# Kernel tuning notes

Hardware: AMD Instinct MI355X
Metric: run time of the kernel (lower is better)

The kernel has to match this reference:

```python
import jax, jax.numpy as jnp
import numpy as np

D_MODEL = 512
D_STATE = 64
HEADDIM = 64
EXPAND = 2
D_CONV = 4
D_INNER = EXPAND * D_MODEL            # 1024
NHEADS = D_INNER // HEADDIM           # 16
CONV_DIM = D_INNER + 2 * D_STATE      # 1152 (x, B, C share the depthwise conv)
D_IN_PROJ = 2 * D_INNER + 2 * D_STATE + NHEADS  # z, xBC, dt
C_IN = 512


def setup_inputs() -> dict:
    key = jax.random.key(0)
    ks = jax.random.split(key, 10)
    hs = jax.random.normal(ks[0], (1, C_IN, 16, 16, 16), jnp.float32)
    return {
        "hidden_states": hs,
        # 1x1 conv projections (weight stored as (out,in))
        "proj_in_w": jax.random.normal(ks[1], (D_MODEL, C_IN), jnp.float32) / np.float32(np.sqrt(C_IN)),
        "proj_in_b": jnp.zeros((D_MODEL,), jnp.float32),
        "proj_out_w": jax.random.normal(ks[2], (C_IN, D_MODEL), jnp.float32) * jnp.float32(0.02),
        "proj_out_b": jnp.zeros((C_IN,), jnp.float32),
        # Mamba2 core params
        "in_proj_w": jax.random.normal(ks[3], (D_IN_PROJ, D_MODEL), jnp.float32) / np.float32(np.sqrt(D_MODEL)),
        "conv_w": jax.random.normal(ks[4], (CONV_DIM, D_CONV), jnp.float32) / np.float32(np.sqrt(D_CONV)),
        "conv_b": jnp.zeros((CONV_DIM,), jnp.float32),
        "dt_bias": jnp.log(jnp.expm1(jax.random.uniform(ks[5], (NHEADS,), jnp.float32, 1e-3, 0.1))),
        "A_log": jnp.log(jax.random.uniform(ks[6], (NHEADS,), jnp.float32, 1.0, 16.0)),
        "D": jnp.ones((NHEADS,), jnp.float32),
        "norm_w": jnp.ones((D_INNER,), jnp.float32),
        "out_proj_w": jax.random.normal(ks[7], (D_MODEL, D_INNER), jnp.float32) / np.float32(np.sqrt(D_INNER)),
    }


def _mamba2(x, in_proj_w, conv_w, conv_b, dt_bias, A_log, Dp, norm_w, out_proj_w):
    # x: (N, T, d_model) with N = B*H*W (independent pixel sequences over time)
    N, T, _ = x.shape
    zxbcdt = jnp.einsum('ntd,ed->nte', x, in_proj_w)  # (N,T,D_IN_PROJ)
    z = zxbcdt[..., :D_INNER]
    xBC = zxbcdt[..., D_INNER:D_INNER + CONV_DIM]
    dt = zxbcdt[..., D_INNER + CONV_DIM:]             # (N,T,NHEADS)
    # causal depthwise conv along T (kernel D_CONV, left-padded), then SiLU
    pad = jnp.pad(xBC, ((0, 0), (D_CONV - 1, 0), (0, 0)))
    xc = sum(pad[:, k:k + T, :] * conv_w[:, k] for k in range(D_CONV))
    xBC = jax.nn.silu(xc + conv_b)
    xs = xBC[..., :D_INNER].reshape(N, T, NHEADS, HEADDIM)
    Bm = xBC[..., D_INNER:D_INNER + D_STATE]          # (N,T,D_STATE), ngroups=1
    Cm = xBC[..., D_INNER + D_STATE:]                 # (N,T,D_STATE)
    dt = jax.nn.softplus(dt + dt_bias)                # (N,T,NHEADS)
    A = -jnp.exp(A_log)                               # (NHEADS,)

    def step(h, inp):
        # h: (N, NHEADS, HEADDIM, D_STATE)
        dt_t, x_t, B_t, C_t = inp
        dA = jnp.exp(dt_t * A)                        # (N,NHEADS)
        h = h * dA[:, :, None, None] + (dt_t[:, :, None] * x_t)[..., None] * B_t[:, None, None, :]
        y_t = jnp.einsum('nhps,ns->nhp', h, C_t)      # (N,NHEADS,HEADDIM)
        return h, y_t

    h0 = jnp.zeros((N, NHEADS, HEADDIM, D_STATE), x.dtype)
    _, ys = jax.lax.scan(step, h0, (dt.swapaxes(0, 1), xs.swapaxes(0, 1), Bm.swapaxes(0, 1), Cm.swapaxes(0, 1)))
    y = ys.swapaxes(0, 1) + Dp[None, None, :, None] * xs   # skip term
    # gated RMSNorm: norm(y * silu(z)) * weight
    y = y.reshape(N, T, D_INNER) * jax.nn.silu(z)
    y = y * jax.lax.rsqrt(jnp.mean(y * y, axis=-1, keepdims=True) + 1e-5) * norm_w
    return jnp.einsum('ntd,od->nto', y, out_proj_w)


def reference(hidden_states, proj_in_w, proj_in_b, proj_out_w, proj_out_b,
              in_proj_w, conv_w, conv_b, dt_bias, A_log, D, norm_w, out_proj_w):
    B, C, T, H, W = hidden_states.shape
    # proj_in: 1x1 conv over channels == per-pixel matmul
    x = jnp.einsum('bcthw,dc->bthwd', hidden_states, proj_in_w) + proj_in_b
    # (B,T,H,W,D) -> (B*H*W, T, D): each pixel becomes a temporal sequence
    x = x.transpose(0, 2, 3, 1, 4).reshape(B * H * W, T, D_MODEL)
    y = _mamba2(x, in_proj_w, conv_w, conv_b, dt_bias, A_log, D, norm_w, out_proj_w)
    y = y.reshape(B, H, W, T, D_MODEL).transpose(0, 3, 1, 2, 4)  # (B,T,H,W,D)
    out = jnp.einsum('bthwd,cd->bcthw', y, proj_out_w) + proj_out_b[None, :, None, None, None]
    return (out,)
```

## Files before the change

### kernel.cpp

```cpp
#include <hip/hip_runtime.h>
#include <hip/hip_bf16.h>
#include <math.h>

#define TT       16
#define NSEQ     256
#define TOK      4096
#define DMODEL   512
#define DINNER   1024
#define DSTATE   64
#define NHEADS   16
#define HEADDIM  64
#define CONVDIM  1152
#define DINPROJ  2192
#define DTOFF    2176
#define ZLD      2176
#define NPAD_IP  2304

using bf16x8 = __attribute__((ext_vector_type(8))) short;
using f32x4  = __attribute__((ext_vector_type(4))) float;
typedef __hip_bfloat16 bf16;

__device__ __forceinline__ void gload_lds16(const void* g, void* l) {
    __builtin_amdgcn_global_load_lds(
        (const __attribute__((address_space(1))) unsigned int*)g,
        (__attribute__((address_space(3))) unsigned int*)l,
        16, 0, 0);
}

template<int NFRAG, bool OUTBF, bool DUAL, int BIAS, bool PARTSCALE, bool COLSCALE>
__global__ __launch_bounds__(256) void mfma_gemm(
    const bf16* __restrict__ A, const bf16* __restrict__ B,
    const float* __restrict__ bias, const float* __restrict__ rs,
    float* __restrict__ Cf, bf16* __restrict__ Ch, float* __restrict__ C2,
    int Nreal, int K, int lda, int ldb, int ldc)
{
    constexpr int BN = NFRAG * 32;
    __shared__ short As[128 * 32];
    __shared__ short Bs[BN * 32];

    const int tid = threadIdx.x;
    const int wv = tid >> 6, ln = tid & 63;
    const int m0 = blockIdx.x * 128, n0 = blockIdx.y * BN;
    const int wr = wv >> 1, wc = wv & 1;
    const int lr = ln & 15, lk = (ln >> 4) * 8;

    f32x4 acc[4][NFRAG];
#pragma unroll
    for (int m = 0; m < 4; ++m)
#pragma unroll
        for (int n = 0; n < NFRAG; ++n) acc[m][n] = (f32x4){0.f, 0.f, 0.f, 0.f};

    for (int k0 = 0; k0 < K; k0 += 32) {
        __syncthreads();
#pragma unroll
        for (int r = 0; r < 2; ++r) {
            const int ofs = r * 4096 + tid * 16;
            const int row = ofs >> 6;
            const int ke  = (ofs & 63) >> 1;
            gload_lds16(A + (size_t)(m0 + row) * lda + k0 + ke, (char*)As + ofs);
        }
#pragma unroll
        for (int r = 0; r < NFRAG / 2; ++r) {
            const int ofs = r * 4096 + tid * 16;
            const int row = ofs >> 6;
            const int ke  = (ofs & 63) >> 1;
            gload_lds16(B + (size_t)(n0 + row) * ldb + k0 + ke, (char*)Bs + ofs);
        }
        __syncthreads();

        bf16x8 af[4], bfr[NFRAG];
#pragma unroll
        for (int m = 0; m < 4; ++m)
            af[m] = *(const bf16x8*)&As[(wr * 64 + m * 16 + lr) * 32 + lk];
#pragma unroll
        for (int n = 0; n < NFRAG; ++n)
            bfr[n] = *(const bf16x8*)&Bs[(wc * (BN / 2) + n * 16 + lr) * 32 + lk];
#pragma unroll
        for (int m = 0; m < 4; ++m)
#pragma unroll
            for (int n = 0; n < NFRAG; ++n)
                acc[m][n] = __builtin_amdgcn_mfma_f32_16x16x32_bf16(
                    af[m], bfr[n], acc[m][n], 0, 0, 0);
    }

    const int mBase = m0 + wr * 64, nBase = n0 + wc * (BN / 2);

    float scn[NFRAG], cbv[NFRAG];
#pragma unroll
    for (int n = 0; n < NFRAG; ++n) {
        const int col = nBase + n * 16 + lr;
        scn[n] = 1.f; cbv[n] = 0.f;
        if (col < Nreal) {
            if (COLSCALE) {
                const float4 pv = *(const float4*)(rs + (size_t)col * 4);
                scn[n] = rsqrtf((pv.x + pv.y + pv.z + pv.w) * (1.f / 1024.f) + 1e-5f);
            }
            if (BIAS == 1) cbv[n] = bias[col];
        }
    }

#pragma unroll
    for (int m = 0; m < 4; ++m) {
#pragma unroll
        for (int j = 0; j < 4; ++j) {
            const int row = mBase + m * 16 + (ln >> 4) * 4 + j;
            float sc = 1.f, rb = 0.f;
            if (PARTSCALE) {
                const float4 pv = *(const float4*)(rs + (size_t)row * 4);
                sc = rsqrtf((pv.x + pv.y + pv.z + pv.w) * (1.f / 1024.f) + 1e-5f);
            }
            if (BIAS == 2) rb = bias[row];
#pragma unroll
            for (int n = 0; n < NFRAG; ++n) {
                const int col = nBase + n * 16 + lr;
                if (col < Nreal) {
                    float v = acc[m][n][j];
                    if (PARTSCALE) v *= sc;
                    if (COLSCALE)  v *= scn[n];
                    v += cbv[n] + rb;
                    if (OUTBF) {
                        Ch[(size_t)row * ldc + col] = __float2bfloat16(v);
                        if (DUAL) C2[(size_t)row * ldc + col] = v;
                    } else {
                        Cf[(size_t)row * ldc + col] = v;
                    }
                }
            }
        }
    }
}

#define SZ_PI  (512 * 512)
#define SZ_PO  (512 * 512)
#define SZ_IP  (DINPROJ * 512)
#define SZ_IPP (NPAD_IP * 512)
#define SZ_ALL (SZ_PI + SZ_PO + SZ_IPP)
#define NB_WC  128
#define NB_WB  768
#define NB_WT  512
#define NB_HT  2048
#define NB_ALL (NB_WC + NB_WB + NB_WT + NB_HT)

__global__ __launch_bounds__(256) void prep_all(
    const float* __restrict__ pi, const float* __restrict__ po,
    const float* __restrict__ op, const float* __restrict__ ip,
    const float* __restrict__ nw, const float* __restrict__ pib,
    const float* __restrict__ hs,
    bf16* __restrict__ wpi, bf16* __restrict__ wpo, bf16* __restrict__ wip,
    bf16* __restrict__ wopT, bf16* __restrict__ hsT,
    float* __restrict__ Wc, float* __restrict__ bc)
{
    __shared__ float smem[32 * 33];
    const int b = blockIdx.x, tid = threadIdx.x;

    if (b < NB_WC) {
        const int h = b >> 3, c0 = (b & 7) * 64;
        const int w = tid >> 6, l = tid & 63;
        const float* wdt = ip + (size_t)(DTOFF + h) * DMODEL;
        float acc = 0.f;
#pragma unroll 8
        for (int i = 0; i < 128; ++i) {
            const int d = w * 128 + i;
            acc = fmaf(wdt[d], pi[(size_t)d * DMODEL + c0 + l], acc);
        }
        smem[w * 64 + l] = acc;
        __syncthreads();
        if (tid < 64)
            Wc[(size_t)h * DMODEL + c0 + tid] =
                smem[tid] + smem[64 + tid] + smem[128 + tid] + smem[192 + tid];
        if ((b & 7) == 0) {
            float p = pib[tid] * wdt[tid] + pib[tid + 256] * wdt[tid + 256];
#pragma unroll
            for (int off = 32; off >= 1; off >>= 1) p += __shfl_xor(p, off);
            if ((tid & 63) == 0) smem[300 + (tid >> 6)] = p;
            __syncthreads();
            if (tid == 0)
                bc[h] = smem[300] + smem[301] + smem[302] + smem[303];
        }
    } else if (b < NB_WC + NB_WB) {
        const int wb = b - NB_WC;
        for (int idx = wb * 256 + tid; idx < SZ_ALL; idx += NB_WB * 256) {
            if (idx < SZ_PI) {
                wpi[idx] = __float2bfloat16(pi[idx]);
            } else if (idx < SZ_PI + SZ_PO) {
                int j = idx - SZ_PI; wpo[j] = __float2bfloat16(po[j]);
            } else {
                int j = idx - SZ_PI - SZ_PO;
                wip[j] = (j < SZ_IP) ? __float2bfloat16(ip[j])
                                     : __float2bfloat16(0.f);
            }
        }
    } else if (b < NB_WC + NB_WB + NB_WT) {
        const int tb = b - NB_WC - NB_WB;
        const int o0 = (tb & 15) * 32, d0 = (tb >> 4) * 32;
        const int tx = tid & 31, ty = tid >> 5;
#pragma unroll
        for (int i = 0; i < 4; ++i)
            smem[(ty + 8 * i) * 33 + tx] =
                op[(size_t)(o0 + ty + 8 * i) * DINNER + d0 + tx];
        __syncthreads();
#pragma unroll
        for (int i = 0; i < 4; ++i) {
            const int d = d0 + ty + 8 * i;
            wopT[(size_t)d * DMODEL + o0 + tx] =
                __float2bfloat16(smem[tx * 33 + ty + 8 * i] * nw[d]);
        }
    } else {
        const int tb = b - NB_WC - NB_WB - NB_WT;
        const int v0 = (tb & 127) * 32, c0 = (tb >> 7) * 32;
        const int tx = tid & 31, ty = tid >> 5;
#pragma unroll
        for (int i = 0; i < 4; ++i)
            smem[(ty + 8 * i) * 33 + tx] =
                hs[(size_t)(c0 + ty + 8 * i) * TOK + v0 + tx];
        __syncthreads();
#pragma unroll
        for (int i = 0; i < 4; ++i)
            hsT[(size_t)(v0 + ty + 8 * i) * DMODEL + c0 + tx] =
                __float2bfloat16(smem[tx * 33 + ty + 8 * i]);
    }
}

__global__ __launch_bounds__(256) void dt_bf_kernel(
    const bf16* __restrict__ hsT, const float* __restrict__ Wc,
    const float* __restrict__ bc, float* __restrict__ dtf)
{
    const int v = blockIdx.x;
    const int w = threadIdx.x >> 6, l = threadIdx.x & 63;

    const bf16x8 hv = *(const bf16x8*)(hsT + (size_t)v * DMODEL + l * 8);
    float hf[8];
#pragma unroll
    for (int j = 0; j < 8; ++j) {
        const unsigned int bits = ((unsigned int)(unsigned short)hv[j]) << 16;
        hf[j] = __uint_as_float(bits);
    }
#pragma unroll
    for (int hh = 0; hh < 4; ++hh) {
        const int h = w * 4 + hh;
        const float4* wr = (const float4*)(Wc + (size_t)h * DMODEL);
        const float4 w0 = wr[l * 2], w1 = wr[l * 2 + 1];
        float dot = hf[0] * w0.x + hf[1] * w0.y + hf[2] * w0.z + hf[3] * w0.w
                  + hf[4] * w1.x + hf[5] * w1.y + hf[6] * w1.z + hf[7] * w1.w;
#pragma unroll
        for (int off = 32; off >= 1; off >>= 1) dot += __shfl_xor(dot, off);
        if (l == 0) dtf[(size_t)v * 16 + h] = dot + bc[h];
    }
}

__global__ __launch_bounds__(256) void ssd_kernel(
    const bf16* __restrict__ zb, const float* __restrict__ dtf,
    const float* __restrict__ conv_w, const float* __restrict__ conv_b,
    const float* __restrict__ dt_bias, const float* __restrict__ A_log,
    const float* __restrict__ Dp,
    bf16* __restrict__ gb, float* __restrict__ part)
{
    const int n = blockIdx.x, hq = blockIdx.y;
    const int tid = threadIdx.x;
    const int w = tid >> 6, p = tid & 63;
    const int h = hq * 4 + w;
    const int ch = hq * 256 + tid;

    __shared__ float Bsh[16][68];
    __shared__ float Csh[16][68];
    __shared__ float Gsh[16][16];
    __shared__ float Msh[4][256];
    __shared__ float red4[16][4];

    float ld[16];
#pragma unroll
    for (int t = 0; t < 16; ++t)
        ld[t] = __bfloat162float(zb[(size_t)(t * 256 + n) * ZLD + 1024 + ch]);

    const float cw0 = conv_w[ch * 4 + 0], cw1 = conv_w[ch * 4 + 1],
                cw2 = conv_w[ch * 4 + 2], cw3 = conv_w[ch * 4 + 3];
    const float cb = conv_b[ch];
    float xs[16];
#pragma unroll
    for (int t = 0; t < 16; ++t) {
        float a = fmaf(ld[t], cw3, cb);
        if (t >= 1) a = fmaf(ld[t - 1], cw2, a);
        if (t >= 2) a = fmaf(ld[t - 2], cw1, a);
        if (t >= 3) a = fmaf(ld[t - 3], cw0, a);
        xs[t] = a / (1.f + __expf(-a));
    }

    if (tid < 128) {
        const int cc = 1024 + tid;
        const float dw0 = conv_w[cc * 4 + 0], dw1 = conv_w[cc * 4 + 1],
                    dw2 = conv_w[cc * 4 + 2], dw3 = conv_w[cc * 4 + 3];
        const float db = conv_b[cc];
        float q0 = 0.f, q1 = 0.f, q2 = 0.f;
#pragma unroll
        for (int t = 0; t < 16; ++t) {
            const float cur =
                __bfloat162float(zb[(size_t)(t * 256 + n) * ZLD + 2048 + tid]);
            float a = fmaf(cur, dw3, db);
            a = fmaf(q2, dw2, a);
            a = fmaf(q1, dw1, a);
            a = fmaf(q0, dw0, a);
            const float val = a / (1.f + __expf(-a));
            if (tid < 64) Bsh[t][tid] = val; else Csh[t][tid - 64] = val;
            q0 = q1; q1 = q2; q2 = cur;
        }
    }

    const float a_h = -__expf(A_log[h]);
    float dtv_l = 0.f;
    if (p < 16) {
        const float raw = dtf[(size_t)(p * 256 + n) * 16 + h] + dt_bias[h];
        dtv_l = (raw > 20.f) ? raw : log1pf(__expf(raw));
    }
    float cum_l = dtv_l;
#pragma unroll
    for (int off = 1; off < 16; off <<= 1) {
        const float tmp = __shfl_up(cum_l, off);
        if (p >= off) cum_l += tmp;
    }
    __syncthreads();

    {
        const int t = tid >> 4, s = tid & 15;
        float acc = 0.f;
#pragma unroll
        for (int k = 0; k < 64; ++k)
            acc = fmaf(Csh[t][k], Bsh[s][k], acc);
        Gsh[t][s] = acc;
    }
    __syncthreads();

    float dtv_all[16], cum_all[16];
#pragma unroll
    for (int t = 0; t < 16; ++t) {
        dtv_all[t] = __shfl(dtv_l, t);
        cum_all[t] = __shfl(cum_l, t);
    }
#pragma unroll
    for (int q = 0; q < 4; ++q) {
        const int idx = p * 4 + q;
        const int t = idx >> 4, s = idx & 15;
        float m = 0.f;
        if (s <= t)
            m = __expf(a_h * (cum_all[t] - cum_all[s])) * Gsh[t][s] * dtv_all[s];
        Msh[w][idx] = m;
    }

    float zl[16];
#pragma unroll
    for (int t = 0; t < 16; ++t)
        zl[t] = __bfloat162float(zb[(size_t)(t * 256 + n) * ZLD + ch]);

    const float Dh = Dp[h];
    float g[16];
#pragma unroll
    for (int t = 0; t < 16; ++t) {
        float y = 0.f;
#pragma unroll
        for (int s = 0; s <= t; ++s)
            y = fmaf(Msh[w][t * 16 + s], xs[s], y);
        y = fmaf(Dh, xs[t], y);
        g[t] = y * (zl[t] / (1.f + __expf(-zl[t])));
    }

#pragma unroll
    for (int t = 0; t < 16; ++t) {
        float ss = g[t] * g[t];
#pragma unroll
        for (int off = 32; off >= 1; off >>= 1) ss += __shfl_xor(ss, off);
        if (p == 0) red4[t][w] = ss;
        gb[(size_t)(t * 256 + n) * DINNER + ch] = __float2bfloat16(g[t]);
    }
    __syncthreads();
    if (tid < 16)
        part[(size_t)(tid * 256 + n) * 4 + hq] =
            red4[tid][0] + red4[tid][1] + red4[tid][2] + red4[tid][3];
}

extern "C" void kernel_launch(void* const* d_in, const int* in_sizes, int n_in,
                              void* d_out, int out_size, void* d_ws, size_t ws_size,
                              hipStream_t stream) {
    const float* hs         = (const float*)d_in[0];
    const float* proj_in_w  = (const float*)d_in[1];
    const float* proj_in_b  = (const float*)d_in[2];
    const float* proj_out_w = (const float*)d_in[3];
    const float* proj_out_b = (const float*)d_in[4];
    const float* in_proj_w  = (const float*)d_in[5];
    const float* conv_w     = (const float*)d_in[6];
    const float* conv_b     = (const float*)d_in[7];
    const float* dt_bias    = (const float*)d_in[8];
    const float* A_log      = (const float*)d_in[9];
    const float* Dp         = (const float*)d_in[10];
    const float* norm_w     = (const float*)d_in[11];
    const float* out_proj_w = (const float*)d_in[12];
    float* out = (float*)d_out;

    float* ws      = (float*)d_ws;
    float* dtf     = ws;
    float* part    = dtf + (size_t)TOK * 16;
    float* Wc      = part + (size_t)TOK * 4;
    float* bc      = Wc + 16 * DMODEL;
    bf16*  hsT     = (bf16*)(bc + 16);
    bf16*  xv_bf   = hsT + (size_t)TOK * DMODEL;
    bf16*  zb      = xv_bf + (size_t)TOK * DMODEL;
    bf16*  gb      = zb + (size_t)TOK * ZLD;
    bf16*  wpi     = gb + (size_t)TOK * DINNER;
    bf16*  wpo     = wpi + SZ_PI;
    bf16*  wip     = wpo + SZ_PO;
    bf16*  wopT    = wip + SZ_IPP;
    bf16*  Wbig    = wopT + (size_t)DINNER * DMODEL;

    prep_all<<<NB_ALL, 256, 0, stream>>>(
        proj_in_w, proj_out_w, out_proj_w, in_proj_w, norm_w, proj_in_b, hs,
        wpi, wpo, wip, wopT, hsT, Wc, bc);

    mfma_gemm<2, true, false, 0, false, false><<<dim3(4, 16), 256, 0, stream>>>(
        wpo, wopT, nullptr, nullptr, nullptr, Wbig, nullptr,
        DINNER, DMODEL, DMODEL, DMODEL, DINNER);

    mfma_gemm<2, true, false, 1, false, false><<<dim3(32, 8), 256, 0, stream>>>(
        hsT, wpi, proj_in_b, nullptr, nullptr, xv_bf, nullptr,
        DMODEL, DMODEL, DMODEL, DMODEL, DMODEL);

    mfma_gemm<4, true, false, 0, false, false><<<dim3(32, 18), 256, 0, stream>>>(
        xv_bf, wip, nullptr, nullptr, nullptr, zb, nullptr,
        ZLD, DMODEL, DMODEL, DMODEL, ZLD);

    dt_bf_kernel<<<TOK, 256, 0, stream>>>(hsT, Wc, bc, dtf);

    ssd_kernel<<<dim3(NSEQ, 4), 256, 0, stream>>>(
        zb, dtf, conv_w, conv_b, dt_bias, A_log, Dp, gb, part);

    mfma_gemm<2, false, false, 2, false, true><<<dim3(4, 64), 256, 0, stream>>>(
        Wbig, gb, proj_out_b, part, out, nullptr, nullptr,
        TOK, DINNER, DINNER, DINNER, TOK);
}
```

Baseline: 121.0 us.

## Merge independent GEMM and dt launches into combined grid kernels

Puts the two independent weight-fold and proj_in GEMMs into one launch, and the in_proj GEMM plus the dt dot-product kernel into another, by dispatching on block index. The final GEMM becomes a specialized non-template kernel, and the in_proj weight padding to 2304 rows is dropped because only the 2176 needed columns are computed. The goal is fewer kernel launches with more concurrent blocks per launch. The trade-off is that the merged kernels share one LDS allocation sized for the larger path, which may lower occupancy for the dt blocks.

Measured after the change: 100.4 us. 17.0% less time.

```diff
diff --git a/kernel.cpp b/kernel.cpp
--- a/kernel.cpp
+++ b/kernel.cpp
@@ -14,7 +14,6 @@
 #define DINPROJ  2192
 #define DTOFF    2176
 #define ZLD      2176
-#define NPAD_IP  2304
 
 using bf16x8 = __attribute__((ext_vector_type(8))) short;
 using f32x4  = __attribute__((ext_vector_type(4))) float;
@@ -27,20 +26,17 @@
         16, 0, 0);
 }
 
-template<int NFRAG, bool OUTBF, bool DUAL, int BIAS, bool PARTSCALE, bool COLSCALE>
-__global__ __launch_bounds__(256) void mfma_gemm(
+template<int NFRAG>
+__device__ __forceinline__ void gemm_core(
+    short* As, short* Bs,
     const bf16* __restrict__ A, const bf16* __restrict__ B,
-    const float* __restrict__ bias, const float* __restrict__ rs,
-    float* __restrict__ Cf, bf16* __restrict__ Ch, float* __restrict__ C2,
-    int Nreal, int K, int lda, int ldb, int ldc)
+    const float* __restrict__ bias, bf16* __restrict__ Ch,
+    int bm, int bn, int K, int lda, int ldb, int ldc, int Nreal)
 {
     constexpr int BN = NFRAG * 32;
-    __shared__ short As[128 * 32];
-    __shared__ short Bs[BN * 32];
-
     const int tid = threadIdx.x;
     const int wv = tid >> 6, ln = tid & 63;
-    const int m0 = blockIdx.x * 128, n0 = blockIdx.y * BN;
+    const int m0 = bm * 128, n0 = bn * BN;
     const int wr = wv >> 1, wc = wv & 1;
     const int lr = ln & 15, lk = (ln >> 4) * 8;
 
@@ -84,47 +80,98 @@
     }
 
     const int mBase = m0 + wr * 64, nBase = n0 + wc * (BN / 2);
-
-    float scn[NFRAG], cbv[NFRAG];
+    float cbv[NFRAG];
 #pragma unroll
     for (int n = 0; n < NFRAG; ++n) {
         const int col = nBase + n * 16 + lr;
-        scn[n] = 1.f; cbv[n] = 0.f;
-        if (col < Nreal) {
-            if (COLSCALE) {
-                const float4 pv = *(const float4*)(rs + (size_t)col * 4);
-                scn[n] = rsqrtf((pv.x + pv.y + pv.z + pv.w) * (1.f / 1024.f) + 1e-5f);
-            }
-            if (BIAS == 1) cbv[n] = bias[col];
-        }
-    }
-
+        cbv[n] = (bias != nullptr && col < Nreal) ? bias[col] : 0.f;
+    }
 #pragma unroll
     for (int m = 0; m < 4; ++m) {
 #pragma unroll
         for (int j = 0; j < 4; ++j) {
             const int row = mBase + m * 16 + (ln >> 4) * 4 + j;
-            float sc = 1.f, rb = 0.f;
-            if (PARTSCALE) {
-                const float4 pv = *(const float4*)(rs + (size_t)row * 4);
-                sc = rsqrtf((pv.x + pv.y + pv.z + pv.w) * (1.f / 1024.f) + 1e-5f);
-            }
-            if (BIAS == 2) rb = bias[row];
 #pragma unroll
             for (int n = 0; n < NFRAG; ++n) {
                 const int col = nBase + n * 16 + lr;
-                if (col < Nreal) {
-                    float v = acc[m][n][j];
-                    if (PARTSCALE) v *= sc;
-                    if (COLSCALE)  v *= scn[n];
-                    v += cbv[n] + rb;
-                    if (OUTBF) {
-                        Ch[(size_t)row * ldc + col] = __float2bfloat16(v);
-                        if (DUAL) C2[(size_t)row * ldc + col] = v;
-                    } else {
-                        Cf[(size_t)row * ldc + col] = v;
-                    }
-                }
+                if (col < Nreal)
+                    Ch[(size_t)row * ldc + col] =
+                        __float2bfloat16(acc[m][n][j] + cbv[n]);
+            }
+        }
+    }
+}
+
+__global__ __launch_bounds__(256) void k67_gemm(
+    const bf16* __restrict__ A, const bf16* __restrict__ B,
+    const float* __restrict__ bias, const float* __restrict__ rs,
+    float* __restrict__ Cf, int K, int lda, int ldb, int ldc)
+{
+    __shared__ short As[128 * 32];
+    __shared__ short Bs[64 * 32];
+
+    const int tid = threadIdx.x;
+    const int wv = tid >> 6, ln = tid & 63;
+    const int m0 = blockIdx.x * 128, n0 = blockIdx.y * 64;
+    const int wr = wv >> 1, wc = wv & 1;
+    const int lr = ln & 15, lk = (ln >> 4) * 8;
+
+    f32x4 acc[4][2];
+#pragma unroll
+    for (int m = 0; m < 4; ++m)
+#pragma unroll
+        for (int n = 0; n < 2; ++n) acc[m][n] = (f32x4){0.f, 0.f, 0.f, 0.f};
+
+    for (int k0 = 0; k0 < K; k0 += 32) {
+        __syncthreads();
+#pragma unroll
+        for (int r = 0; r < 2; ++r) {
+            const int ofs = r * 4096 + tid * 16;
+            const int row = ofs >> 6;
+            const int ke  = (ofs & 63) >> 1;
+            gload_lds16(A + (size_t)(m0 + row) * lda + k0 + ke, (char*)As + ofs);
+        }
+        {
+            const int ofs = tid * 16;
+            const int row = ofs >> 6;
+            const int ke  = (ofs & 63) >> 1;
+            gload_lds16(B + (size_t)(n0 + row) * ldb + k0 + ke, (char*)Bs + ofs);
+        }
+        __syncthreads();
+
+        bf16x8 af[4], bfr[2];
+#pragma unroll
+        for (int m = 0; m < 4; ++m)
+            af[m] = *(const bf16x8*)&As[(wr * 64 + m * 16 + lr) * 32 + lk];
+#pragma unroll
+        for (int n = 0; n < 2; ++n)
+            bfr[n] = *(const bf16x8*)&Bs[(wc * 32 + n * 16 + lr) * 32 + lk];
+#pragma unroll
+        for (int m = 0; m < 4; ++m)
+#pragma unroll
+            for (int n = 0; n < 2; ++n)
+                acc[m][n] = __builtin_amdgcn_mfma_f32_16x16x32_bf16(
+                    af[m], bfr[n], acc[m][n], 0, 0, 0);
+    }
+
+    const int mBase = m0 + wr * 64, nBase = n0 + wc * 32;
+    float scn[2];
+#pragma unroll
+    for (int n = 0; n < 2; ++n) {
+        const int col = nBase + n * 16 + lr;
+        const float4 pv = *(const float4*)(rs + (size_t)col * 4);
+        scn[n] = rsqrtf((pv.x + pv.y + pv.z + pv.w) * (1.f / 1024.f) + 1e-5f);
+    }
+#pragma unroll
+    for (int m = 0; m < 4; ++m) {
+#pragma unroll
+        for (int j = 0; j < 4; ++j) {
+            const int row = mBase + m * 16 + (ln >> 4) * 4 + j;
+            const float rb = bias[row];
+#pragma unroll
+            for (int n = 0; n < 2; ++n) {
+                const int col = nBase + n * 16 + lr;
+                Cf[(size_t)row * ldc + col] = acc[m][n][j] * scn[n] + rb;
             }
         }
     }
@@ -132,9 +179,8 @@
 
 #define SZ_PI  (512 * 512)
 #define SZ_PO  (512 * 512)
-#define SZ_IP  (DINPROJ * 512)
-#define SZ_IPP (NPAD_IP * 512)
-#define SZ_ALL (SZ_PI + SZ_PO + SZ_IPP)
+#define SZ_IP2 (ZLD * 512)
+#define SZ_ALL (SZ_PI + SZ_PO + SZ_IP2)
 #define NB_WC  128
 #define NB_WB  768
 #define NB_WT  512
@@ -186,8 +232,7 @@
                 int j = idx - SZ_PI; wpo[j] = __float2bfloat16(po[j]);
             } else {
                 int j = idx - SZ_PI - SZ_PO;
-                wip[j] = (j < SZ_IP) ? __float2bfloat16(ip[j])
-                                     : __float2bfloat16(0.f);
+                wip[j] = __float2bfloat16(ip[j]);
             }
         }
     } else if (b < NB_WC + NB_WB + NB_WT) {
@@ -221,30 +266,58 @@
     }
 }
 
-__global__ __launch_bounds__(256) void dt_bf_kernel(
+__global__ __launch_bounds__(256) void gemm_p2k1(
+    const bf16* __restrict__ wpo, const bf16* __restrict__ wopT,
+    const bf16* __restrict__ hsT, const bf16* __restrict__ wpi,
+    const float* __restrict__ pib,
+    bf16* __restrict__ Wbig, bf16* __restrict__ xv_bf)
+{
+    __shared__ short As[128 * 32];
+    __shared__ short Bs[64 * 32];
+    const int b = blockIdx.x;
+    if (b < 64) {
+        gemm_core<2>(As, Bs, wpo, wopT, nullptr, Wbig,
+                     b & 3, b >> 2, DMODEL, DMODEL, DMODEL, DINNER, DINNER);
+    } else {
+        const int b2 = b - 64;
+        gemm_core<2>(As, Bs, hsT, wpi, pib, xv_bf,
+                     b2 & 31, b2 >> 5, DMODEL, DMODEL, DMODEL, DMODEL, DMODEL);
+    }
+}
+
+__global__ __launch_bounds__(256) void k2_dt(
+    const bf16* __restrict__ xv_bf, const bf16* __restrict__ wip,
     const bf16* __restrict__ hsT, const float* __restrict__ Wc,
-    const float* __restrict__ bc, float* __restrict__ dtf)
+    const float* __restrict__ bc,
+    bf16* __restrict__ zb, float* __restrict__ dtf)
 {
-    const int v = blockIdx.x;
-    const int w = threadIdx.x >> 6, l = threadIdx.x & 63;
-
-    const bf16x8 hv = *(const bf16x8*)(hsT + (size_t)v * DMODEL + l * 8);
-    float hf[8];
-#pragma unroll
-    for (int j = 0; j < 8; ++j) {
-        const unsigned int bits = ((unsigned int)(unsigned short)hv[j]) << 16;
-        hf[j] = __uint_as_float(bits);
-    }
-#pragma unroll
-    for (int hh = 0; hh < 4; ++hh) {
-        const int h = w * 4 + hh;
-        const float4* wr = (const float4*)(Wc + (size_t)h * DMODEL);
-        const float4 w0 = wr[l * 2], w1 = wr[l * 2 + 1];
-        float dot = hf[0] * w0.x + hf[1] * w0.y + hf[2] * w0.z + hf[3] * w0.w
-                  + hf[4] * w1.x + hf[5] * w1.y + hf[6] * w1.z + hf[7] * w1.w;
-#pragma unroll
-        for (int off = 32; off >= 1; off >>= 1) dot += __shfl_xor(dot, off);
-        if (l == 0) dtf[(size_t)v * 16 + h] = dot + bc[h];
+    __shared__ short As[128 * 32];
+    __shared__ short Bs[128 * 32];
+    const int b = blockIdx.x;
+    if (b < 544) {
+        gemm_core<4>(As, Bs, xv_bf, wip, nullptr, zb,
+                     b & 31, b >> 5, DMODEL, DMODEL, DMODEL, ZLD, ZLD);
+    } else {
+        const int v = b - 544;
+        const int w = threadIdx.x >> 6, l = threadIdx.x & 63;
+        const bf16x8 hv = *(const bf16x8*)(hsT + (size_t)v * DMODEL + l * 8);
+        float hf[8];
+#pragma unroll
+        for (int j = 0; j < 8; ++j) {
+            const unsigned int bits = ((unsigned int)(unsigned short)hv[j]) << 16;
+            hf[j] = __uint_as_float(bits);
+        }
+#pragma unroll
+        for (int hh = 0; hh < 4; ++hh) {
+            const int h = w * 4 + hh;
+            const float4* wr = (const float4*)(Wc + (size_t)h * DMODEL);
+            const float4 w0 = wr[l * 2], w1 = wr[l * 2 + 1];
+            float dot = hf[0] * w0.x + hf[1] * w0.y + hf[2] * w0.z + hf[3] * w0.w
+                      + hf[4] * w1.x + hf[5] * w1.y + hf[6] * w1.z + hf[7] * w1.w;
+#pragma unroll
+            for (int off = 32; off >= 1; off >>= 1) dot += __shfl_xor(dot, off);
+            if (l == 0) dtf[(size_t)v * 16 + h] = dot + bc[h];
+        }
     }
 }
 
@@ -406,31 +479,22 @@
     bf16*  wpi     = gb + (size_t)TOK * DINNER;
     bf16*  wpo     = wpi + SZ_PI;
     bf16*  wip     = wpo + SZ_PO;
-    bf16*  wopT    = wip + SZ_IPP;
+    bf16*  wopT    = wip + SZ_IP2;
     bf16*  Wbig    = wopT + (size_t)DINNER * DMODEL;
 
     prep_all<<<NB_ALL, 256, 0, stream>>>(
         proj_in_w, proj_out_w, out_proj_w, in_proj_w, norm_w, proj_in_b, hs,
         wpi, wpo, wip, wopT, hsT, Wc, bc);
 
-    mfma_gemm<2, true, false, 0, false, false><<<dim3(4, 16), 256, 0, stream>>>(
-        wpo, wopT, nullptr, nullptr, nullptr, Wbig, nullptr,
-        DINNER, DMODEL, DMODEL, DMODEL, DINNER);
-
-    mfma_gemm<2, true, false, 1, false, false><<<dim3(32, 8), 256, 0, stream>>>(
-        hsT, wpi, proj_in_b, nullptr, nullptr, xv_bf, nullptr,
-        DMODEL, DMODEL, DMODEL, DMODEL, DMODEL);
-
-    mfma_gemm<4, true, false, 0, false, false><<<dim3(32, 18), 256, 0, stream>>>(
-        xv_bf, wip, nullptr, nullptr, nullptr, zb, nullptr,
-        ZLD, DMODEL, DMODEL, DMODEL, ZLD);
-
-    dt_bf_kernel<<<TOK, 256, 0, stream>>>(hsT, Wc, bc, dtf);
+    gemm_p2k1<<<320, 256, 0, stream>>>(
+        wpo, wopT, hsT, wpi, proj_in_b, Wbig, xv_bf);
+
+    k2_dt<<<544 + TOK, 256, 0, stream>>>(
+        xv_bf, wip, hsT, Wc, bc, zb, dtf);
 
     ssd_kernel<<<dim3(NSEQ, 4), 256, 0, stream>>>(
         zb, dtf, conv_w, conv_b, dt_bias, A_log, Dp, gb, part);
 
-    mfma_gemm<2, false, false, 2, false, true><<<dim3(4, 64), 256, 0, stream>>>(
-        Wbig, gb, proj_out_b, part, out, nullptr, nullptr,
-        TOK, DINNER, DINNER, DINNER, TOK);
-}
+    k67_gemm<<<dim3(4, 64), 256, 0, stream>>>(
+        Wbig, gb, proj_out_b, part, out, DINNER, DINNER, DINNER, TOK);
+}
```
